# Performance work log

Hardware: AMD Instinct MI355X
Metric: run time of the kernel (lower is better)

Reference implementation:

```python
import jax, jax.numpy as jnp
import numpy as np

A = 5.0  # smoothness parameter from init_kwargs


def setup_inputs() -> dict:
    key = jax.random.key(0)
    k1, k2 = jax.random.split(key)
    x = jax.random.uniform(k1, (512, 512), dtype=jnp.float32)        # [B, in_features]
    weight = jax.random.uniform(k2, (512, 1024), dtype=jnp.float32)  # [in_features, out_features]
    return {"x": x, "weight": weight}


def reference(x, weight):
    # inner[b, i, o] = max(x[b, i], weight[i, o])
    inner = jnp.maximum(x[..., :, None], weight[None])  # [B, I, O]
    # hard min over in_features
    hard = jnp.min(inner, axis=-2)                       # [B, O]
    # smooth (log-sum-exp) soft-min over in_features
    smooth = -jax.nn.logsumexp(-A * inner, axis=-2) / A  # [B, O]
    # STE: forward value == hard, gradient flows through smooth
    return hard - jax.lax.stop_gradient(smooth) + smooth
```

## Files before the change

### kernel.cpp

```cpp
#include <hip/hip_runtime.h>


#define B_DIM 512
#define I_DIM 512
#define O_DIM 1024
#define NBUCK 256

#define RL(v_, l_) ((unsigned)__builtin_amdgcn_readlane((int)(v_), (l_)))

__global__ __launch_bounds__(1024, 8) void SmoothSTEMinMax_fused(
    const float* __restrict__ x,
    const float* __restrict__ w,
    float* __restrict__ out) {
  __shared__ unsigned int hist[NBUCK];
  __shared__ unsigned int wssum[4];
  __shared__ unsigned int sdat[2 * I_DIM];

  const int t = threadIdx.x;
  const int b = blockIdx.x;
  const int lane = t & 63;

  float xval = 0.0f;
  int bb = 0;
  if (t < I_DIM) {
    xval = x[b * I_DIM + t];
    bb = (int)(xval * 256.0f);
    bb = bb > 255 ? 255 : (bb < 0 ? 0 : bb);
  }
  if (t < NBUCK) hist[t] = 0;
  __syncthreads();
  if (t < I_DIM) atomicAdd(&hist[bb], 1u);
  __syncthreads();

  unsigned v = 0, cnt = 0;
  if (t < NBUCK) {
    cnt = hist[t];
    v = cnt;
#pragma unroll
    for (int d = 1; d < 64; d <<= 1) {
      const unsigned n = __shfl_up(v, d, 64);
      if (lane >= d) v += n;
    }
    if (lane == 63) wssum[t >> 6] = v;
  }
  __syncthreads();
  if (t < NBUCK) {
    unsigned add = 0;
#pragma unroll
    for (int ww = 0; ww < 4; ++ww)
      if (ww < (t >> 6)) add += wssum[ww];
    hist[t] = v + add - cnt;
  }
  __syncthreads();
  if (t < I_DIM) {
    const unsigned pos = atomicAdd(&hist[bb], 1u);
    sdat[2 * pos] = (unsigned)t * (unsigned)(O_DIM * 4);
    sdat[2 * pos + 1] = __float_as_uint(xval);
  }
  __syncthreads();

  const unsigned o4 = (unsigned)t * 4u;
  const char* wb = reinterpret_cast<const char*>(w);
  float A = 3.402823466e+38f;

  const uint4 q = *reinterpret_cast<const uint4*>(&sdat[4 * lane]);

#pragma unroll
  for (int c = 0; c < 8; ++c) {
    float wv[8], xv[8];
#pragma unroll
    for (int e = 0; e < 8; ++e) {
      const int g = c * 8 + e;
      const unsigned off = RL((g & 1) ? q.z : q.x, g >> 1);
      const unsigned xb  = RL((g & 1) ? q.w : q.y, g >> 1);
      xv[e] = __uint_as_float(xb);
      wv[e] = *reinterpret_cast<const float*>(wb + (off + o4));
    }
#pragma unroll
    for (int e = 0; e < 8; ++e) A = fminf(A, fmaxf(xv[e], wv[e]));
  }

  int k = 64;
#pragma unroll
  for (int c = 8; c < 16; ++c) {
    const float nx = __uint_as_float(RL(q.y, 4 * c));
    const float th = (float)(int)(nx * 256.0f) * 0.00390625f;
    if (!__any(A > th)) break;
#pragma unroll
    for (int e = 0; e < 8; ++e) {
      const int g = c * 8 + e;
      const unsigned off = RL((g & 1) ? q.z : q.x, g >> 1);
      const unsigned xb  = RL((g & 1) ? q.w : q.y, g >> 1);
      const float wvv = *reinterpret_cast<const float*>(wb + (off + o4));
      A = fminf(A, fmaxf(__uint_as_float(xb), wvv));
    }
    k += 8;
  }

  if (k >= 128) {
    while (k < I_DIM) {
      const float nx = __uint_as_float(
          (unsigned)__builtin_amdgcn_readfirstlane((int)sdat[2 * k + 1]));
      const float th = (float)(int)(nx * 256.0f) * 0.00390625f;
      if (!__any(A > th)) break;
#pragma unroll
      for (int u = 0; u < 8; ++u) {
        const unsigned off =
            (unsigned)__builtin_amdgcn_readfirstlane((int)sdat[2 * (k + u)]);
        const unsigned xb =
            (unsigned)__builtin_amdgcn_readfirstlane((int)sdat[2 * (k + u) + 1]);
        const float wvv = *reinterpret_cast<const float*>(wb + (off + o4));
        A = fminf(A, fmaxf(__uint_as_float(xb), wvv));
      }
      k += 8;
    }
  }

  out[b * O_DIM + t] = A;
}

extern "C" void kernel_launch(void* const* d_in, const int* in_sizes, int n_in,
                              void* d_out, int out_size, void* d_ws, size_t ws_size,
                              hipStream_t stream) {
  const float* x = (const float*)d_in[0];
  const float* w = (const float*)d_in[1];
  float* out = (float*)d_out;

  SmoothSTEMinMax_fused<<<B_DIM, 1024, 0, stream>>>(x, w, out);
}
```

Before: 13.62 us.

## Process two batch rows per block with float2 weight loads per thread

Each block now handles two batch rows. Each thread covers two adjacent output columns and loads them with 8-byte vector loads, and the sort/histogram stage runs for both rows in parallel across all 1024 threads. This halves the number of blocks and raises per-thread work so that weight loads are wider and the setup cost is amortized. The trade-off is that early exit is now decided over two accumulators per lane, which may make waves continue longer, and only 256 blocks are launched, which lowers parallelism.

```diff
diff --git a/kernel.cpp b/kernel.cpp
--- a/kernel.cpp
+++ b/kernel.cpp
@@ -7,77 +7,87 @@
 #define NBUCK 256
 
 #define RL(v_, l_) ((unsigned)__builtin_amdgcn_readlane((int)(v_), (l_)))
+#define RFL(v_) ((unsigned)__builtin_amdgcn_readfirstlane((int)(v_)))
+
+typedef float float2v __attribute__((ext_vector_type(2)));
 
 __global__ __launch_bounds__(1024, 8) void SmoothSTEMinMax_fused(
     const float* __restrict__ x,
     const float* __restrict__ w,
     float* __restrict__ out) {
-  __shared__ unsigned int hist[NBUCK];
-  __shared__ unsigned int wssum[4];
-  __shared__ unsigned int sdat[2 * I_DIM];
+  __shared__ unsigned int hist[2][NBUCK];
+  __shared__ unsigned int wssum[2][4];
+  __shared__ uint2 sdat[2][I_DIM];
 
   const int t = threadIdx.x;
-  const int b = blockIdx.x;
+  const int blk = blockIdx.x;
   const int lane = t & 63;
+  const int r = t >> 9;
+  const int idx = t & 511;
 
-  float xval = 0.0f;
-  int bb = 0;
-  if (t < I_DIM) {
-    xval = x[b * I_DIM + t];
-    bb = (int)(xval * 256.0f);
-    bb = bb > 255 ? 255 : (bb < 0 ? 0 : bb);
-  }
-  if (t < NBUCK) hist[t] = 0;
+  const float xval = x[(2 * blk + r) * I_DIM + idx];
+  int bb = (int)(xval * 256.0f);
+  bb = bb > 255 ? 255 : (bb < 0 ? 0 : bb);
+  if (t < 512) hist[t >> 8][t & 255] = 0;
   __syncthreads();
-  if (t < I_DIM) atomicAdd(&hist[bb], 1u);
+  atomicAdd(&hist[r][bb], 1u);
   __syncthreads();
 
   unsigned v = 0, cnt = 0;
-  if (t < NBUCK) {
-    cnt = hist[t];
+  if (t < 512) {
+    cnt = hist[t >> 8][t & 255];
     v = cnt;
 #pragma unroll
     for (int d = 1; d < 64; d <<= 1) {
       const unsigned n = __shfl_up(v, d, 64);
       if (lane >= d) v += n;
     }
-    if (lane == 63) wssum[t >> 6] = v;
+    if (lane == 63) wssum[t >> 8][(t & 255) >> 6] = v;
   }
   __syncthreads();
-  if (t < NBUCK) {
+  if (t < 512) {
     unsigned add = 0;
 #pragma unroll
     for (int ww = 0; ww < 4; ++ww)
-      if (ww < (t >> 6)) add += wssum[ww];
-    hist[t] = v + add - cnt;
+      if (ww < ((t & 255) >> 6)) add += wssum[t >> 8][ww];
+    hist[t >> 8][t & 255] = v + add - cnt;
   }
   __syncthreads();
-  if (t < I_DIM) {
-    const unsigned pos = atomicAdd(&hist[bb], 1u);
-    sdat[2 * pos] = (unsigned)t * (unsigned)(O_DIM * 4);
-    sdat[2 * pos + 1] = __float_as_uint(xval);
+  {
+    const unsigned pos = atomicAdd(&hist[r][bb], 1u);
+    sdat[r][pos] = make_uint2((unsigned)idx * (unsigned)(O_DIM * 4),
+                              __float_as_uint(xval));
   }
   __syncthreads();
 
-  const unsigned o4 = (unsigned)t * 4u;
+  const int wv_ = t >> 6;
+  const int br = wv_ >> 3;
+  const int sl = wv_ & 7;
+  const int orow = 2 * blk + br;
   const char* wb = reinterpret_cast<const char*>(w);
-  float A = 3.402823466e+38f;
+  const unsigned o8 = (unsigned)(sl * 128 + lane * 2) * 4u;
 
-  const uint4 q = *reinterpret_cast<const uint4*>(&sdat[4 * lane]);
+  const uint4 q = *reinterpret_cast<const uint4*>(&sdat[br][2 * lane]);
+
+  float A0 = 3.402823466e+38f, A1 = A0;
 
 #pragma unroll
   for (int c = 0; c < 8; ++c) {
-    float wv[8], xv[8];
+    float2v wv2[8];
+    float xv[8];
 #pragma unroll
     for (int e = 0; e < 8; ++e) {
       const int g = c * 8 + e;
       const unsigned off = RL((g & 1) ? q.z : q.x, g >> 1);
       const unsigned xb  = RL((g & 1) ? q.w : q.y, g >> 1);
       xv[e] = __uint_as_float(xb);
-      wv[e] = *reinterpret_cast<const float*>(wb + (off + o4));
+      wv2[e] = *reinterpret_cast<const float2v*>(wb + (off + o8));
     }
 #pragma unroll
-    for (int e = 0; e < 8; ++e) A = fminf(A, fmaxf(xv[e], wv[e]));
+    for (int e = 0; e < 8; ++e) {
+      A0 = fminf(A0, fmaxf(xv[e], wv2[e].x));
+      A1 = fminf(A1, fmaxf(xv[e], wv2[e].y));
+    }
   }
 
   int k = 64;
@@ -85,38 +95,40 @@
   for (int c = 8; c < 16; ++c) {
     const float nx = __uint_as_float(RL(q.y, 4 * c));
     const float th = (float)(int)(nx * 256.0f) * 0.00390625f;
-    if (!__any(A > th)) break;
+    if (!__any(A0 > th || A1 > th)) break;
 #pragma unroll
     for (int e = 0; e < 8; ++e) {
       const int g = c * 8 + e;
       const unsigned off = RL((g & 1) ? q.z : q.x, g >> 1);
       const unsigned xb  = RL((g & 1) ? q.w : q.y, g >> 1);
-      const float wvv = *reinterpret_cast<const float*>(wb + (off + o4));
-      A = fminf(A, fmaxf(__uint_as_float(xb), wvv));
+      const float2v wvv = *reinterpret_cast<const float2v*>(wb + (off + o8));
+      A0 = fminf(A0, fmaxf(__uint_as_float(xb), wvv.x));
+      A1 = fminf(A1, fmaxf(__uint_as_float(xb), wvv.y));
     }
     k += 8;
   }
 
   if (k >= 128) {
     while (k < I_DIM) {
-      const float nx = __uint_as_float(
-          (unsigned)__builtin_amdgcn_readfirstlane((int)sdat[2 * k + 1]));
+      const float nx = __uint_as_float(RFL(sdat[br][k].y));
       const float th = (float)(int)(nx * 256.0f) * 0.00390625f;
-      if (!__any(A > th)) break;
+      if (!__any(A0 > th || A1 > th)) break;
 #pragma unroll
       for (int u = 0; u < 8; ++u) {
-        const unsigned off =
-            (unsigned)__builtin_amdgcn_readfirstlane((int)sdat[2 * (k + u)]);
-        const unsigned xb =
-            (unsigned)__builtin_amdgcn_readfirstlane((int)sdat[2 * (k + u) + 1]);
-        const float wvv = *reinterpret_cast<const float*>(wb + (off + o4));
-        A = fminf(A, fmaxf(__uint_as_float(xb), wvv));
+        const unsigned off = RFL(sdat[br][k + u].x);
+        const unsigned xb  = RFL(sdat[br][k + u].y);
+        const float2v wvv = *reinterpret_cast<const float2v*>(wb + (off + o8));
+        A0 = fminf(A0, fmaxf(__uint_as_float(xb), wvv.x));
+        A1 = fminf(A1, fmaxf(__uint_as_float(xb), wvv.y));
       }
       k += 8;
     }
   }
 
-  out[b * O_DIM + t] = A;
+  float2v res;
+  res.x = A0;
+  res.y = A1;
+  *reinterpret_cast<float2v*>(&out[orow * O_DIM + sl * 128 + lane * 2]) = res;
 }
 
 extern "C" void kernel_launch(void* const* d_in, const int* in_sizes, int n_in,
@@ -126,5 +138,5 @@
   const float* w = (const float*)d_in[1];
   float* out = (float*)d_out;
 
-  SmoothSTEMinMax_fused<<<B_DIM, 1024, 0, stream>>>(x, w, out);
+  SmoothSTEMinMax_fused<<<B_DIM / 2, 1024, 0, stream>>>(x, w, out);
 }
```

After: 15.22 us. +11.7%, slower.

## Split output columns across 256-thread blocks and shrink histogram to 64 buckets

Applied to the files above, without the earlier changes.

Launches a 2D grid of 512x4 blocks with 256 threads each, so every block covers a quarter of the output columns rather than all 1024. Each thread loads two x values, and the counting sort uses 64 buckets, which lets the prefix scan fit in one wavefront and drops one barrier. The cost is that the sort over x is repeated four times per row, and the coarser buckets give looser early-exit thresholds, which may let more waves keep scanning candidates.

```diff
diff --git a/kernel.cpp b/kernel.cpp
--- a/kernel.cpp
+++ b/kernel.cpp
@@ -4,66 +4,57 @@
 #define B_DIM 512
 #define I_DIM 512
 #define O_DIM 1024
-#define NBUCK 256
+#define NBUCK 64
 
 #define RL(v_, l_) ((unsigned)__builtin_amdgcn_readlane((int)(v_), (l_)))
+#define RFL(v_) ((unsigned)__builtin_amdgcn_readfirstlane((int)(v_)))
 
-__global__ __launch_bounds__(1024, 8) void SmoothSTEMinMax_fused(
+__global__ __launch_bounds__(256, 8) void SmoothSTEMinMax_fused(
     const float* __restrict__ x,
     const float* __restrict__ w,
     float* __restrict__ out) {
   __shared__ unsigned int hist[NBUCK];
-  __shared__ unsigned int wssum[4];
-  __shared__ unsigned int sdat[2 * I_DIM];
+  __shared__ uint2 sdat[I_DIM];
 
   const int t = threadIdx.x;
   const int b = blockIdx.x;
   const int lane = t & 63;
 
-  float xval = 0.0f;
-  int bb = 0;
-  if (t < I_DIM) {
-    xval = x[b * I_DIM + t];
-    bb = (int)(xval * 256.0f);
-    bb = bb > 255 ? 255 : (bb < 0 ? 0 : bb);
-  }
+  const float xv0 = x[b * I_DIM + t];
+  const float xv1 = x[b * I_DIM + 256 + t];
+  int b0 = (int)(xv0 * 64.0f); b0 = b0 > 63 ? 63 : (b0 < 0 ? 0 : b0);
+  int b1 = (int)(xv1 * 64.0f); b1 = b1 > 63 ? 63 : (b1 < 0 ? 0 : b1);
+
   if (t < NBUCK) hist[t] = 0;
   __syncthreads();
-  if (t < I_DIM) atomicAdd(&hist[bb], 1u);
+  atomicAdd(&hist[b0], 1u);
+  atomicAdd(&hist[b1], 1u);
   __syncthreads();
-
-  unsigned v = 0, cnt = 0;
   if (t < NBUCK) {
-    cnt = hist[t];
-    v = cnt;
+    const unsigned cnt = hist[t];
+    unsigned v = cnt;
 #pragma unroll
     for (int d = 1; d < 64; d <<= 1) {
       const unsigned n = __shfl_up(v, d, 64);
       if (lane >= d) v += n;
     }
-    if (lane == 63) wssum[t >> 6] = v;
+    hist[t] = v - cnt;
   }
   __syncthreads();
-  if (t < NBUCK) {
-    unsigned add = 0;
-#pragma unroll
-    for (int ww = 0; ww < 4; ++ww)
-      if (ww < (t >> 6)) add += wssum[ww];
-    hist[t] = v + add - cnt;
-  }
-  __syncthreads();
-  if (t < I_DIM) {
-    const unsigned pos = atomicAdd(&hist[bb], 1u);
-    sdat[2 * pos] = (unsigned)t * (unsigned)(O_DIM * 4);
-    sdat[2 * pos + 1] = __float_as_uint(xval);
+  {
+    const unsigned p0 = atomicAdd(&hist[b0], 1u);
+    sdat[p0] = make_uint2((unsigned)t * (unsigned)(O_DIM * 4), __float_as_uint(xv0));
+    const unsigned p1 = atomicAdd(&hist[b1], 1u);
+    sdat[p1] = make_uint2((unsigned)(t + 256) * (unsigned)(O_DIM * 4),
+                          __float_as_uint(xv1));
   }
   __syncthreads();
 
-  const unsigned o4 = (unsigned)t * 4u;
+  const unsigned o4 = (unsigned)(blockIdx.y * 256 + t) * 4u;
   const char* wb = reinterpret_cast<const char*>(w);
   float A = 3.402823466e+38f;
 
-  const uint4 q = *reinterpret_cast<const uint4*>(&sdat[4 * lane]);
+  const uint4 q = *reinterpret_cast<const uint4*>(&sdat[2 * lane]);
 
 #pragma unroll
   for (int c = 0; c < 8; ++c) {
@@ -84,7 +75,7 @@
 #pragma unroll
   for (int c = 8; c < 16; ++c) {
     const float nx = __uint_as_float(RL(q.y, 4 * c));
-    const float th = (float)(int)(nx * 256.0f) * 0.00390625f;
+    const float th = (float)(int)(nx * 64.0f) * 0.015625f;
     if (!__any(A > th)) break;
 #pragma unroll
     for (int e = 0; e < 8; ++e) {
@@ -99,16 +90,13 @@
 
   if (k >= 128) {
     while (k < I_DIM) {
-      const float nx = __uint_as_float(
-          (unsigned)__builtin_amdgcn_readfirstlane((int)sdat[2 * k + 1]));
-      const float th = (float)(int)(nx * 256.0f) * 0.00390625f;
+      const float nx = __uint_as_float(RFL(sdat[k].y));
+      const float th = (float)(int)(nx * 64.0f) * 0.015625f;
       if (!__any(A > th)) break;
 #pragma unroll
       for (int u = 0; u < 8; ++u) {
-        const unsigned off =
-            (unsigned)__builtin_amdgcn_readfirstlane((int)sdat[2 * (k + u)]);
-        const unsigned xb =
-            (unsigned)__builtin_amdgcn_readfirstlane((int)sdat[2 * (k + u) + 1]);
+        const unsigned off = RFL(sdat[k + u].x);
+        const unsigned xb  = RFL(sdat[k + u].y);
         const float wvv = *reinterpret_cast<const float*>(wb + (off + o4));
         A = fminf(A, fmaxf(__uint_as_float(xb), wvv));
       }
@@ -116,7 +104,7 @@
     }
   }
 
-  out[b * O_DIM + t] = A;
+  out[b * O_DIM + blockIdx.y * 256 + t] = A;
 }
 
 extern "C" void kernel_launch(void* const* d_in, const int* in_sizes, int n_in,
@@ -126,5 +114,6 @@
   const float* w = (const float*)d_in[1];
   float* out = (float*)d_out;
 
-  SmoothSTEMinMax_fused<<<B_DIM, 1024, 0, stream>>>(x, w, out);
+  dim3 grid(B_DIM, O_DIM / 256);
+  SmoothSTEMinMax_fused<<<grid, 256, 0, stream>>>(x, w, out);
 }
```

Result: slower. 13.91 us (+2.1%).
